# Optimization experiments

Hardware: AMD Instinct MI355X
Metric: run time of the kernel (lower is better)

Reference implementation:

```python
import jax, jax.numpy as jnp
import numpy as np

V = 100000
EMB = 300      # embedding_dim / output_dim
H1 = 100       # h1_dim
H2 = 100       # h2_dim
PROD = 100     # prod_dim
B = 16384


def setup_inputs() -> dict:
    key = jax.random.key(0)
    ks = jax.random.split(key, 16)
    targets = jax.random.randint(ks[0], (B,), 0, V)
    contexts = jax.random.randint(ks[1], (B,), 0, V)
    times = jax.random.uniform(ks[2], (B,), dtype=jnp.float32)
    labels = jax.random.randint(ks[3], (B,), 0, 2).astype(jnp.float32)
    # learned parameters
    targetemb = jax.random.normal(ks[4], (V, EMB), dtype=jnp.float32) * 0.02
    contextemb = jax.random.normal(ks[5], (V, EMB), dtype=jnp.float32) * 0.02
    # h1 initialized per the RANDA/RANDB scheme in __init__
    rng = np.random.RandomState(0)
    randoffset = rng.rand(H1, 1)
    randa = (1.0 / np.sqrt(2.0)) * rng.randn(H1, 1)
    randb = (-1.0 * randoffset * randa).reshape((H1,))
    h1_k = jnp.asarray(randa.reshape(1, H1), dtype=jnp.float32)
    h1_b = jnp.asarray(randb, dtype=jnp.float32)
    h2_k = jax.random.normal(ks[6], (H1, H2), dtype=jnp.float32) * 0.1
    h2_b = jnp.zeros((H2,), dtype=jnp.float32)
    evoke_k = jax.random.normal(ks[7], (EMB, H2 * PROD), dtype=jnp.float32) * 0.05
    evoke_b = jnp.zeros((H2 * PROD,), dtype=jnp.float32)
    last_k = jax.random.normal(ks[8], (PROD, EMB), dtype=jnp.float32) * 0.1
    last_b = jnp.zeros((EMB,), dtype=jnp.float32)
    return {
        "targets": targets, "contexts": contexts, "times": times, "labels": labels,
        "targetemb": targetemb, "contextemb": contextemb,
        "h1_k": h1_k, "h1_b": h1_b, "h2_k": h2_k, "h2_b": h2_b,
        "evoke_k": evoke_k, "evoke_b": evoke_b, "last_k": last_k, "last_b": last_b,
    }


def _branch_vector(emb, tv, evoke_k, evoke_b, last_k, last_b):
    # emb: [B, EMB] gathered embeddings; tv: [B, H2] time vector
    mat = (emb @ evoke_k + evoke_b).reshape(-1, PROD, H2)   # [B, PROD, H2]
    mv = jnp.einsum('bph,bh->bp', mat, tv)                   # batched matvec
    return mv @ last_k + last_b                              # [B, EMB]


def reference(targets, contexts, times, labels, targetemb, contextemb,
              h1_k, h1_b, h2_k, h2_b, evoke_k, evoke_b, last_k, last_b):
    # time MLP: two tanh dense layers (intended h1 -> h2 stack)
    t = times.reshape(-1, 1)
    h1 = jnp.tanh(t @ h1_k + h1_b)          # [B, H1]
    tv = jnp.tanh(h1 @ h2_k + h2_b)         # [B, H2]
    targ_vect = _branch_vector(targetemb[targets], tv, evoke_k, evoke_b, last_k, last_b)
    cont_vect = _branch_vector(contextemb[contexts], tv, evoke_k, evoke_b, last_k, last_b)
    logits = jnp.sum(targ_vect * cont_vect, axis=1)  # [B]
    # sigmoid_cross_entropy_with_logits, numerically stable
    loss = jnp.maximum(logits, 0.0) - logits * labels + jnp.log1p(jnp.exp(-jnp.abs(logits)))
    return jnp.mean(loss)
```

## Files before the change

### kernel.cpp

```cpp
#include <hip/hip_runtime.h>
#include <cstdint>

#define VOCAB 100000
#define EMB 300
#define NE 301
#define KP 128
#define EKSTRIDE 28672
#define NP 128
#define BM 64
#define BTOT 16384
#define PSZ 112
#define NGRP 4

typedef __attribute__((ext_vector_type(8))) short short8;
typedef __attribute__((ext_vector_type(4))) float f32x4;

__device__ __forceinline__ unsigned short f2bf(float f) {
    uint32_t u = __float_as_uint(f);
    uint32_t r = (u + 0x7fffu + ((u >> 16) & 1u)) >> 16;
    return (unsigned short)r;
}

__global__ __launch_bounds__(256) void k_ekprep(const float* __restrict__ evoke_k,
                                                const float* __restrict__ evoke_b,
                                                unsigned short* __restrict__ ekp) {
    int e = blockIdx.x;
    const float* src = (e < EMB) ? (evoke_k + (size_t)e * 10000) : evoke_b;
    uint32_t* dst = (uint32_t*)(ekp + (size_t)e * (EKSTRIDE / 2));
#pragma unroll
    for (int it = 0; it < 7; ++it) {
        int c    = it * 256 + threadIdx.x;
        int lane = c & 63;
        int ks   = (c >> 6) & 3;
        int t    = c >> 8;
        int p    = t * 16 + (lane & 15);
        int h0   = ks * 32 + (lane >> 4) * 8;
        uint32_t ov[4] = {0u, 0u, 0u, 0u};
        if (p < 100) {
#pragma unroll
            for (int j = 0; j < 8; ++j) {
                int h = h0 + j;
                float f = (h < 100) ? src[p * 100 + h] : 0.f;
                ov[j >> 1] |= (uint32_t)f2bf(f) << ((j & 1) * 16);
            }
        }
        uint32_t* o = dst + (size_t)c * 4;
        o[0] = ov[0]; o[1] = ov[1]; o[2] = ov[2]; o[3] = ov[3];
    }
}

__global__ __launch_bounds__(256) void k_tv(const float* __restrict__ times,
                                            const float* __restrict__ h1_k,
                                            const float* __restrict__ h1_b,
                                            const float* __restrict__ h2_k,
                                            const float* __restrict__ h2_b,
                                            unsigned short* __restrict__ tvp) {
    __shared__ float h1s[16][100];
    int b0 = blockIdx.x * 16;
    for (int idx = threadIdx.x; idx < 1600; idx += 256) {
        int bb = idx / 100, i = idx - bb * 100;
        h1s[bb][i] = tanhf(times[b0 + bb] * h1_k[i] + h1_b[i]);
    }
    __syncthreads();
    for (int idx = threadIdx.x; idx < 1600; idx += 256) {
        int bb = idx / 100, j = idx - bb * 100;
        float acc = h2_b[j];
        for (int i = 0; i < 100; ++i) acc += h1s[bb][i] * h2_k[i * 100 + j];
        tvp[(size_t)(b0 + bb) * KP + j] = f2bf(tanhf(acc));
    }
    for (int idx = threadIdx.x; idx < 16 * 28; idx += 256) {
        int bb = idx / 28, j = 100 + (idx - bb * 28);
        tvp[(size_t)(b0 + bb) * KP + j] = 0;
    }
}

__global__ __launch_bounds__(128) void k_gprep(const float* __restrict__ last_k,
                                               const float* __restrict__ last_b,
                                               float* __restrict__ G,
                                               float* __restrict__ vvec,
                                               float* __restrict__ c0,
                                               float* __restrict__ out) {
    int p = blockIdx.x;
    int q = threadIdx.x;
    __shared__ float row[EMB];
    for (int d = q; d < EMB; d += 128) row[d] = (p < 100) ? last_k[p * EMB + d] : 0.f;
    __syncthreads();
    float acc = 0.f;
    if (p < 100 && q < 100) {
        for (int d = 0; d < EMB; ++d) acc += row[d] * last_k[q * EMB + d];
    }
    G[p * NP + q] = acc;
    if (q == 0) {
        float a = 0.f;
        if (p < 100) {
            for (int d = 0; d < EMB; ++d) a += row[d] * last_b[d];
        }
        vvec[p] = a;
        if (p == 0) {
            float s = 0.f;
            for (int d = 0; d < EMB; ++d) s += last_b[d] * last_b[d];
            *c0 = s;
            *out = 0.f;
        }
    }
}

__global__ __launch_bounds__(256, 2) void k_main(
    const int* __restrict__ targets, const int* __restrict__ contexts,
    const float* __restrict__ targetemb, const float* __restrict__ contextemb,
    const unsigned short* __restrict__ ekp, const unsigned short* __restrict__ tvp,
    float* __restrict__ mvpt, float* __restrict__ mvpc) {
    extern __shared__ char smem[];

    const int tid  = threadIdx.x;
    const int lane = tid & 63;
    const int w    = tid >> 6;
    const int l15  = lane & 15;
    const int l4   = lane >> 4;
    const int low3 = blockIdx.x & 7;
    const int g    = low3 >> 1;
    const int bt   = ((blockIdx.x >> 3) << 1) | (low3 & 1);
    const int m0   = bt * BM;
    const int e0   = (g == 0) ? 0 : (1 + 75 * g);
    const int ecnt = (g == 0) ? 76 : 75;
    const int nreal= (g == 3) ? 74 : ecnt;

    unsigned short* embl = (unsigned short*)smem;

    short8 afrag[4][4];
#pragma unroll
    for (int mt = 0; mt < 4; ++mt) {
        int bg = m0 + mt * 16 + l15;
#pragma unroll
        for (int ks = 0; ks < 4; ++ks) {
            afrag[mt][ks] = *(const short8*)(tvp + (size_t)bg * KP + ks * 32 + l4 * 8);
        }
    }

    bool act[2];
    int  voff[2];
#pragma unroll
    for (int nt = 0; nt < 2; ++nt) {
        int t = w * 2 + nt;
        act[nt] = (t < 7);
        int tc = (t < 7) ? t : 6;
        voff[nt] = tc * 4096 + lane * 16;
    }

    auto issue = [&](short8 (&buf)[2][4], int el) {
        int eg = e0 + ((el < ecnt) ? el : (ecnt - 1));
        uint64_t base = (uint64_t)(const void*)ekp + (uint64_t)eg * EKSTRIDE;
#pragma unroll
        for (int nt = 0; nt < 2; ++nt) {
            asm volatile("global_load_dwordx4 %0, %1, %2 offset:0"
                         : "=v"(buf[nt][0]) : "v"(voff[nt]), "s"(base));
            asm volatile("global_load_dwordx4 %0, %1, %2 offset:1024"
                         : "=v"(buf[nt][1]) : "v"(voff[nt]), "s"(base));
            asm volatile("global_load_dwordx4 %0, %1, %2 offset:2048"
                         : "=v"(buf[nt][2]) : "v"(voff[nt]), "s"(base));
            asm volatile("global_load_dwordx4 %0, %1, %2 offset:3072"
                         : "=v"(buf[nt][3]) : "v"(voff[nt]), "s"(base));
        }
    };
#define WAIT8 do { asm volatile("s_waitcnt vmcnt(8)"); \
                   __builtin_amdgcn_sched_barrier(0); } while (0)
#define WAIT0 do { asm volatile("s_waitcnt vmcnt(0)"); \
                   __builtin_amdgcn_sched_barrier(0); } while (0)

    short8 bufA[2][4], bufB[2][4];
    issue(bufA, 0);
    issue(bufB, 1);

    {
        int off    = tid & 127;
        int b      = off & 63;
        int branch = off >> 6;
        int seg    = tid >> 7;
        int s0 = seg * 38;
        int s1 = (seg == 0) ? 38 : nreal;
        const int* idxp   = branch ? contexts : targets;
        const float* base = branch ? contextemb : targetemb;
        const float* row  = base + (size_t)idxp[m0 + b] * EMB + e0;
        int e = s0;
        for (; e + 3 < s1; e += 4) {
            float4 v = *(const float4*)(row + e);
            embl[(e + 0) * 128 + off] = f2bf(v.x);
            embl[(e + 1) * 128 + off] = f2bf(v.y);
            embl[(e + 2) * 128 + off] = f2bf(v.z);
            embl[(e + 3) * 128 + off] = f2bf(v.w);
        }
        for (; e < s1; ++e) embl[e * 128 + off] = f2bf(row[e]);
        if (g == 3 && seg == 1) embl[74 * 128 + off] = 0x3F80;
    }

    f32x4 acc_t[4][2], acc_c[4][2];
    const f32x4 zf = {0.f, 0.f, 0.f, 0.f};
#pragma unroll
    for (int mt = 0; mt < 4; ++mt) {
#pragma unroll
        for (int nt = 0; nt < 2; ++nt) { acc_t[mt][nt] = zf; acc_c[mt][nt] = zf; }
    }

    auto compute = [&](int el, short8 (&buf)[2][4]) {
        float et[4][4], ec[4][4];
#pragma unroll
        for (int mt = 0; mt < 4; ++mt) {
            int row0 = mt * 16 + l4 * 4;
            uint2 dt = *(const uint2*)(embl + el * 128 + row0);
            uint2 dc = *(const uint2*)(embl + el * 128 + 64 + row0);
            et[mt][0] = __uint_as_float(dt.x << 16);
            et[mt][1] = __uint_as_float(dt.x & 0xffff0000u);
            et[mt][2] = __uint_as_float(dt.y << 16);
            et[mt][3] = __uint_as_float(dt.y & 0xffff0000u);
            ec[mt][0] = __uint_as_float(dc.x << 16);
            ec[mt][1] = __uint_as_float(dc.x & 0xffff0000u);
            ec[mt][2] = __uint_as_float(dc.y << 16);
            ec[mt][3] = __uint_as_float(dc.y & 0xffff0000u);
        }
#pragma unroll
        for (int nt = 0; nt < 2; ++nt) {
            if (act[nt]) {
                f32x4 S[4];
#pragma unroll
                for (int mt = 0; mt < 4; ++mt) S[mt] = zf;
#pragma unroll
                for (int ks = 0; ks < 4; ++ks) {
#pragma unroll
                    for (int mt = 0; mt < 4; ++mt) {
                        S[mt] = __builtin_amdgcn_mfma_f32_16x16x32_bf16(
                            afrag[mt][ks], buf[nt][ks], S[mt], 0, 0, 0);
                    }
                }
#pragma unroll
                for (int mt = 0; mt < 4; ++mt) {
#pragma unroll
                    for (int r = 0; r < 4; ++r) {
                        acc_t[mt][nt][r] += et[mt][r] * S[mt][r];
                        acc_c[mt][nt][r] += ec[mt][r] * S[mt][r];
                    }
                }
            }
        }
    };

    __syncthreads();

    const int ITER = (ecnt - 2) >> 1;
#pragma unroll 1
    for (int i = 0; i < ITER; ++i) {
        int e = 2 * i;
        WAIT8;
        compute(e, bufA);
        issue(bufA, e + 2);
        WAIT8;
        compute(e + 1, bufB);
        issue(bufB, e + 3);
    }
    {
        int e2 = 2 * ITER;
        WAIT0;
        compute(e2, bufA);
        compute(e2 + 1, bufB);
        if (ecnt & 1) {
            issue(bufA, e2 + 2);
            WAIT0;
            compute(e2 + 2, bufA);
        }
    }

    float* ot = mvpt + (size_t)g * BTOT * PSZ;
    float* oc = mvpc + (size_t)g * BTOT * PSZ;
#pragma unroll
    for (int mt = 0; mt < 4; ++mt) {
#pragma unroll
        for (int nt = 0; nt < 2; ++nt) {
            if (act[nt]) {
                int col = (w * 2 + nt) * 16 + l15;
#pragma unroll
                for (int r = 0; r < 4; ++r) {
                    size_t row = m0 + mt * 16 + l4 * 4 + r;
                    ot[row * PSZ + col] = acc_t[mt][nt][r];
                    oc[row * PSZ + col] = acc_c[mt][nt][r];
                }
            }
        }
    }
}

__global__ __launch_bounds__(256) void k_fin(
    const float* __restrict__ labels,
    const float* __restrict__ G, const float* __restrict__ vvec,
    const float* __restrict__ c0p,
    const float* __restrict__ mvpt, const float* __restrict__ mvpc,
    float* __restrict__ out) {
    __shared__ float mvt[32 * PSZ];
    __shared__ float mvc[32 * PSZ];
    __shared__ float bsum[4];
    const int tid = threadIdx.x;
    const int m0  = blockIdx.x * 32;

    for (int idx = tid; idx < 32 * (PSZ / 4); idx += 256) {
        float4 st = make_float4(0.f, 0.f, 0.f, 0.f);
        float4 sc = make_float4(0.f, 0.f, 0.f, 0.f);
#pragma unroll
        for (int gg = 0; gg < NGRP; ++gg) {
            const float4* pt = (const float4*)(mvpt + (size_t)gg * BTOT * PSZ) +
                               (size_t)m0 * (PSZ / 4) + idx;
            const float4* pc = (const float4*)(mvpc + (size_t)gg * BTOT * PSZ) +
                               (size_t)m0 * (PSZ / 4) + idx;
            float4 a = *pt, b = *pc;
            st.x += a.x; st.y += a.y; st.z += a.z; st.w += a.w;
            sc.x += b.x; sc.y += b.y; sc.z += b.z; sc.w += b.w;
        }
        ((float4*)mvt)[idx] = st;
        ((float4*)mvc)[idx] = sc;
    }
    __syncthreads();

    int b_loc = tid >> 3;
    int oct   = tid & 7;
    const float4* Mrow = (const float4*)(mvc + b_loc * PSZ);

    float part = 0.f;
    for (int pp = 0; pp < 14; ++pp) {
        int p = oct * 14 + pp;
        const float4* Grow = (const float4*)(G + p * NP);
        float wq = 0.f;
#pragma unroll 7
        for (int qq = 0; qq < 28; ++qq) {
            float4 gg = Grow[qq];
            float4 m  = Mrow[qq];
            wq += gg.x * m.x + gg.y * m.y + gg.z * m.z + gg.w * m.w;
        }
        float mtv = mvt[b_loc * PSZ + p];
        float mcv = mvc[b_loc * PSZ + p];
        part += mtv * wq + vvec[p] * (mtv + mcv);
    }
    part += __shfl_xor(part, 1);
    part += __shfl_xor(part, 2);
    part += __shfl_xor(part, 4);

    float lossv = 0.f;
    if (oct == 0) {
        float logit = part + *c0p;
        float lab = labels[m0 + b_loc];
        lossv = fmaxf(logit, 0.f) - logit * lab + log1pf(expf(-fabsf(logit)));
    }
#pragma unroll
    for (int off = 8; off < 64; off <<= 1) lossv += __shfl_xor(lossv, off);
    int w = tid >> 6;
    if ((tid & 63) == 0) bsum[w] = lossv;
    __syncthreads();
    if (tid == 0) {
        atomicAdd(out, (bsum[0] + bsum[1] + bsum[2] + bsum[3]) * (1.0f / 16384.0f));
    }
}

extern "C" void kernel_launch(void* const* d_in, const int* in_sizes, int n_in,
                              void* d_out, int out_size, void* d_ws, size_t ws_size,
                              hipStream_t stream) {
    const int*   targets    = (const int*)d_in[0];
    const int*   contexts   = (const int*)d_in[1];
    const float* times      = (const float*)d_in[2];
    const float* labels     = (const float*)d_in[3];
    const float* targetemb  = (const float*)d_in[4];
    const float* contextemb = (const float*)d_in[5];
    const float* h1_k       = (const float*)d_in[6];
    const float* h1_b       = (const float*)d_in[7];
    const float* h2_k       = (const float*)d_in[8];
    const float* h2_b       = (const float*)d_in[9];
    const float* evoke_k    = (const float*)d_in[10];
    const float* evoke_b    = (const float*)d_in[11];
    const float* last_k     = (const float*)d_in[12];
    const float* last_b     = (const float*)d_in[13];
    float* out = (float*)d_out;

    char* ws = (char*)d_ws;
    unsigned short* ekp = (unsigned short*)ws;
    unsigned short* tvp = (unsigned short*)(ws + 8630272);
    float* G    = (float*)(ws + 8630272 + 4194304);
    float* vv   = (float*)(ws + 8630272 + 4194304 + 65536);
    float* c0   = (float*)(ws + 8630272 + 4194304 + 65536 + 512);
    float* mvpt = (float*)(ws + 8630272 + 4194304 + 65536 + 1024);
    float* mvpc = mvpt + (size_t)NGRP * BTOT * PSZ;

    k_ekprep<<<dim3(NE), dim3(256), 0, stream>>>(evoke_k, evoke_b, ekp);
    k_tv<<<dim3(BTOT / 16), dim3(256), 0, stream>>>(times, h1_k, h1_b, h2_k, h2_b, tvp);
    k_gprep<<<dim3(NP), dim3(128), 0, stream>>>(last_k, last_b, G, vv, c0, out);
    k_main<<<dim3(NGRP * BTOT / BM), dim3(256), 19456, stream>>>(
        targets, contexts, targetemb, contextemb, ekp, tvp, mvpt, mvpc);
    k_fin<<<dim3(BTOT / 32), dim3(256), 0, stream>>>(
        labels, G, vv, c0, mvpt, mvpc, out);
}
```

Baseline: 518.5 us.

## Merge prep kernels into one launch, stage G in LDS for finalize

Folds the three preprocessing kernels (evoke_k bf16 packing, time-MLP, last_k Gram matrix) into a single launch that dispatches on block index, saving two kernel launches. The finalize kernel now copies the Gram matrix into padded shared memory and handles 16 batch rows per block with 16 lanes per row, so G is no longer read from global memory inside the loop. The sched_barrier masks in the main kernel are relaxed to let the compiler move some instructions across the wait points. The cost is a large dynamic LDS allocation in finalize, about 65 KB per block, and each of its 1024 blocks reloads the full G.

```diff
diff --git a/kernel.cpp b/kernel.cpp
--- a/kernel.cpp
+++ b/kernel.cpp
@@ -11,6 +11,8 @@
 #define BTOT 16384
 #define PSZ 112
 #define NGRP 4
+#define FSB 16
+#define NPREP (NE + BTOT / 16 + 128)
 
 typedef __attribute__((ext_vector_type(8))) short short8;
 typedef __attribute__((ext_vector_type(4))) float f32x4;
@@ -21,86 +23,86 @@
     return (unsigned short)r;
 }
 
-__global__ __launch_bounds__(256) void k_ekprep(const float* __restrict__ evoke_k,
-                                                const float* __restrict__ evoke_b,
-                                                unsigned short* __restrict__ ekp) {
-    int e = blockIdx.x;
-    const float* src = (e < EMB) ? (evoke_k + (size_t)e * 10000) : evoke_b;
-    uint32_t* dst = (uint32_t*)(ekp + (size_t)e * (EKSTRIDE / 2));
-#pragma unroll
-    for (int it = 0; it < 7; ++it) {
-        int c    = it * 256 + threadIdx.x;
-        int lane = c & 63;
-        int ks   = (c >> 6) & 3;
-        int t    = c >> 8;
-        int p    = t * 16 + (lane & 15);
-        int h0   = ks * 32 + (lane >> 4) * 8;
-        uint32_t ov[4] = {0u, 0u, 0u, 0u};
-        if (p < 100) {
-#pragma unroll
-            for (int j = 0; j < 8; ++j) {
-                int h = h0 + j;
-                float f = (h < 100) ? src[p * 100 + h] : 0.f;
-                ov[j >> 1] |= (uint32_t)f2bf(f) << ((j & 1) * 16);
+__global__ __launch_bounds__(256) void k_prep(
+    const float* __restrict__ evoke_k, const float* __restrict__ evoke_b,
+    unsigned short* __restrict__ ekp,
+    const float* __restrict__ times,
+    const float* __restrict__ h1_k, const float* __restrict__ h1_b,
+    const float* __restrict__ h2_k, const float* __restrict__ h2_b,
+    unsigned short* __restrict__ tvp,
+    const float* __restrict__ last_k, const float* __restrict__ last_b,
+    float* __restrict__ G, float* __restrict__ vvec,
+    float* __restrict__ c0, float* __restrict__ out) {
+    __shared__ float h1s[16][100];
+    __shared__ float row[EMB];
+    const int b = blockIdx.x;
+
+    if (b < NE) {
+        int e = b;
+        const float* src = (e < EMB) ? (evoke_k + (size_t)e * 10000) : evoke_b;
+        uint32_t* dst = (uint32_t*)(ekp + (size_t)e * (EKSTRIDE / 2));
+#pragma unroll
+        for (int it = 0; it < 7; ++it) {
+            int c    = it * 256 + threadIdx.x;
+            int lane = c & 63;
+            int ks   = (c >> 6) & 3;
+            int t    = c >> 8;
+            int p    = t * 16 + (lane & 15);
+            int h0   = ks * 32 + (lane >> 4) * 8;
+            uint32_t ov[4] = {0u, 0u, 0u, 0u};
+            if (p < 100) {
+#pragma unroll
+                for (int j = 0; j < 8; ++j) {
+                    int h = h0 + j;
+                    float f = (h < 100) ? src[p * 100 + h] : 0.f;
+                    ov[j >> 1] |= (uint32_t)f2bf(f) << ((j & 1) * 16);
+                }
             }
-        }
-        uint32_t* o = dst + (size_t)c * 4;
-        o[0] = ov[0]; o[1] = ov[1]; o[2] = ov[2]; o[3] = ov[3];
-    }
-}
-
-__global__ __launch_bounds__(256) void k_tv(const float* __restrict__ times,
-                                            const float* __restrict__ h1_k,
-                                            const float* __restrict__ h1_b,
-                                            const float* __restrict__ h2_k,
-                                            const float* __restrict__ h2_b,
-                                            unsigned short* __restrict__ tvp) {
-    __shared__ float h1s[16][100];
-    int b0 = blockIdx.x * 16;
-    for (int idx = threadIdx.x; idx < 1600; idx += 256) {
-        int bb = idx / 100, i = idx - bb * 100;
-        h1s[bb][i] = tanhf(times[b0 + bb] * h1_k[i] + h1_b[i]);
-    }
-    __syncthreads();
-    for (int idx = threadIdx.x; idx < 1600; idx += 256) {
-        int bb = idx / 100, j = idx - bb * 100;
-        float acc = h2_b[j];
-        for (int i = 0; i < 100; ++i) acc += h1s[bb][i] * h2_k[i * 100 + j];
-        tvp[(size_t)(b0 + bb) * KP + j] = f2bf(tanhf(acc));
-    }
-    for (int idx = threadIdx.x; idx < 16 * 28; idx += 256) {
-        int bb = idx / 28, j = 100 + (idx - bb * 28);
-        tvp[(size_t)(b0 + bb) * KP + j] = 0;
-    }
-}
-
-__global__ __launch_bounds__(128) void k_gprep(const float* __restrict__ last_k,
-                                               const float* __restrict__ last_b,
-                                               float* __restrict__ G,
-                                               float* __restrict__ vvec,
-                                               float* __restrict__ c0,
-                                               float* __restrict__ out) {
-    int p = blockIdx.x;
-    int q = threadIdx.x;
-    __shared__ float row[EMB];
-    for (int d = q; d < EMB; d += 128) row[d] = (p < 100) ? last_k[p * EMB + d] : 0.f;
-    __syncthreads();
-    float acc = 0.f;
-    if (p < 100 && q < 100) {
-        for (int d = 0; d < EMB; ++d) acc += row[d] * last_k[q * EMB + d];
-    }
-    G[p * NP + q] = acc;
-    if (q == 0) {
-        float a = 0.f;
-        if (p < 100) {
-            for (int d = 0; d < EMB; ++d) a += row[d] * last_b[d];
-        }
-        vvec[p] = a;
-        if (p == 0) {
-            float s = 0.f;
-            for (int d = 0; d < EMB; ++d) s += last_b[d] * last_b[d];
-            *c0 = s;
-            *out = 0.f;
+            uint32_t* o = dst + (size_t)c * 4;
+            o[0] = ov[0]; o[1] = ov[1]; o[2] = ov[2]; o[3] = ov[3];
+        }
+    } else if (b < NE + BTOT / 16) {
+        int b0 = (b - NE) * 16;
+        for (int idx = threadIdx.x; idx < 1600; idx += 256) {
+            int bb = idx / 100, i = idx - bb * 100;
+            h1s[bb][i] = tanhf(times[b0 + bb] * h1_k[i] + h1_b[i]);
+        }
+        __syncthreads();
+        for (int idx = threadIdx.x; idx < 1600; idx += 256) {
+            int bb = idx / 100, j = idx - bb * 100;
+            float acc = h2_b[j];
+            for (int i = 0; i < 100; ++i) acc += h1s[bb][i] * h2_k[i * 100 + j];
+            tvp[(size_t)(b0 + bb) * KP + j] = f2bf(tanhf(acc));
+        }
+        for (int idx = threadIdx.x; idx < 16 * 28; idx += 256) {
+            int bb = idx / 28, j = 100 + (idx - bb * 28);
+            tvp[(size_t)(b0 + bb) * KP + j] = 0;
+        }
+    } else {
+        int p = b - NE - BTOT / 16;
+        int q = threadIdx.x;
+        for (int d = threadIdx.x; d < EMB; d += 256)
+            row[d] = (p < 100) ? last_k[p * EMB + d] : 0.f;
+        __syncthreads();
+        if (q < 128) {
+            float acc = 0.f;
+            if (p < 100 && q < 100) {
+                for (int d = 0; d < EMB; ++d) acc += row[d] * last_k[q * EMB + d];
+            }
+            G[p * NP + q] = acc;
+            if (q == 0) {
+                float a = 0.f;
+                if (p < 100) {
+                    for (int d = 0; d < EMB; ++d) a += row[d] * last_b[d];
+                }
+                vvec[p] = a;
+                if (p == 0) {
+                    float s = 0.f;
+                    for (int d = 0; d < EMB; ++d) s += last_b[d] * last_b[d];
+                    *c0 = s;
+                    *out = 0.f;
+                }
+            }
         }
     }
 }
@@ -163,9 +165,9 @@
         }
     };
 #define WAIT8 do { asm volatile("s_waitcnt vmcnt(8)"); \
-                   __builtin_amdgcn_sched_barrier(0); } while (0)
+                   __builtin_amdgcn_sched_barrier(0x387); } while (0)
 #define WAIT0 do { asm volatile("s_waitcnt vmcnt(0)"); \
-                   __builtin_amdgcn_sched_barrier(0); } while (0)
+                   __builtin_amdgcn_sched_barrier(0x387); } while (0)
 
     short8 bufA[2][4], bufB[2][4];
     issue(bufA, 0);
@@ -287,72 +289,77 @@
     }
 }
 
-__global__ __launch_bounds__(256) void k_fin(
+__global__ __launch_bounds__(256, 2) void k_fin(
     const float* __restrict__ labels,
     const float* __restrict__ G, const float* __restrict__ vvec,
     const float* __restrict__ c0p,
     const float* __restrict__ mvpt, const float* __restrict__ mvpc,
     float* __restrict__ out) {
-    __shared__ float mvt[32 * PSZ];
-    __shared__ float mvc[32 * PSZ];
-    __shared__ float bsum[4];
+    extern __shared__ float fs[];
+    float* Gs   = fs;
+    float* mts  = fs + 112 * 116;
+    float* mcs  = mts + FSB * PSZ;
+    float* vs   = mcs + FSB * PSZ;
+    float* lred = vs + PSZ;
     const int tid = threadIdx.x;
-    const int m0  = blockIdx.x * 32;
-
-    for (int idx = tid; idx < 32 * (PSZ / 4); idx += 256) {
+    const int m0  = blockIdx.x * FSB;
+
+    for (int idx = tid; idx < 112 * 28; idx += 256) {
+        int p = idx / 28, qq = idx - p * 28;
+        *(float4*)(Gs + p * 116 + qq * 4) = *(const float4*)(G + p * NP + qq * 4);
+    }
+    for (int idx = tid; idx < FSB * 28; idx += 256) {
+        int s = idx / 28, qq = idx - s * 28;
+        size_t base = (size_t)(m0 + s) * PSZ + qq * 4;
         float4 st = make_float4(0.f, 0.f, 0.f, 0.f);
         float4 sc = make_float4(0.f, 0.f, 0.f, 0.f);
 #pragma unroll
         for (int gg = 0; gg < NGRP; ++gg) {
-            const float4* pt = (const float4*)(mvpt + (size_t)gg * BTOT * PSZ) +
-                               (size_t)m0 * (PSZ / 4) + idx;
-            const float4* pc = (const float4*)(mvpc + (size_t)gg * BTOT * PSZ) +
-                               (size_t)m0 * (PSZ / 4) + idx;
-            float4 a = *pt, b = *pc;
+            float4 a = *(const float4*)(mvpt + (size_t)gg * BTOT * PSZ + base);
+            float4 c = *(const float4*)(mvpc + (size_t)gg * BTOT * PSZ + base);
             st.x += a.x; st.y += a.y; st.z += a.z; st.w += a.w;
-            sc.x += b.x; sc.y += b.y; sc.z += b.z; sc.w += b.w;
-        }
-        ((float4*)mvt)[idx] = st;
-        ((float4*)mvc)[idx] = sc;
-    }
+            sc.x += c.x; sc.y += c.y; sc.z += c.z; sc.w += c.w;
+        }
+        *(float4*)(mts + s * PSZ + qq * 4) = st;
+        *(float4*)(mcs + s * PSZ + qq * 4) = sc;
+    }
+    if (tid < PSZ) vs[tid] = vvec[tid];
     __syncthreads();
 
-    int b_loc = tid >> 3;
-    int oct   = tid & 7;
-    const float4* Mrow = (const float4*)(mvc + b_loc * PSZ);
-
+    const int s = tid >> 4;
+    const int l = tid & 15;
     float part = 0.f;
-    for (int pp = 0; pp < 14; ++pp) {
-        int p = oct * 14 + pp;
-        const float4* Grow = (const float4*)(G + p * NP);
+#pragma unroll 1
+    for (int k = 0; k < 7; ++k) {
+        int p = l * 7 + k;
+        const float4* Gr = (const float4*)(Gs + p * 116);
+        const float4* Mr = (const float4*)(mcs + s * PSZ);
         float wq = 0.f;
-#pragma unroll 7
+#pragma unroll
         for (int qq = 0; qq < 28; ++qq) {
-            float4 gg = Grow[qq];
-            float4 m  = Mrow[qq];
-            wq += gg.x * m.x + gg.y * m.y + gg.z * m.z + gg.w * m.w;
-        }
-        float mtv = mvt[b_loc * PSZ + p];
-        float mcv = mvc[b_loc * PSZ + p];
-        part += mtv * wq + vvec[p] * (mtv + mcv);
+            float4 g = Gr[qq];
+            float4 m = Mr[qq];
+            wq += g.x * m.x + g.y * m.y + g.z * m.z + g.w * m.w;
+        }
+        float mtv = mts[s * PSZ + p];
+        float mcv = mcs[s * PSZ + p];
+        part += mtv * wq + vs[p] * (mtv + mcv);
     }
     part += __shfl_xor(part, 1);
     part += __shfl_xor(part, 2);
     part += __shfl_xor(part, 4);
-
-    float lossv = 0.f;
-    if (oct == 0) {
+    part += __shfl_xor(part, 8);
+    if (l == 0) {
         float logit = part + *c0p;
-        float lab = labels[m0 + b_loc];
-        lossv = fmaxf(logit, 0.f) - logit * lab + log1pf(expf(-fabsf(logit)));
-    }
-#pragma unroll
-    for (int off = 8; off < 64; off <<= 1) lossv += __shfl_xor(lossv, off);
-    int w = tid >> 6;
-    if ((tid & 63) == 0) bsum[w] = lossv;
+        float lab = labels[m0 + s];
+        lred[s] = fmaxf(logit, 0.f) - logit * lab + log1pf(expf(-fabsf(logit)));
+    }
     __syncthreads();
     if (tid == 0) {
-        atomicAdd(out, (bsum[0] + bsum[1] + bsum[2] + bsum[3]) * (1.0f / 16384.0f));
+        float sum = 0.f;
+#pragma unroll
+        for (int i = 0; i < FSB; ++i) sum += lred[i];
+        atomicAdd(out, sum * (1.0f / 16384.0f));
     }
 }
 
@@ -384,11 +391,11 @@
     float* mvpt = (float*)(ws + 8630272 + 4194304 + 65536 + 1024);
     float* mvpc = mvpt + (size_t)NGRP * BTOT * PSZ;
 
-    k_ekprep<<<dim3(NE), dim3(256), 0, stream>>>(evoke_k, evoke_b, ekp);
-    k_tv<<<dim3(BTOT / 16), dim3(256), 0, stream>>>(times, h1_k, h1_b, h2_k, h2_b, tvp);
-    k_gprep<<<dim3(NP), dim3(128), 0, stream>>>(last_k, last_b, G, vv, c0, out);
+    k_prep<<<dim3(NPREP), dim3(256), 0, stream>>>(
+        evoke_k, evoke_b, ekp, times, h1_k, h1_b, h2_k, h2_b, tvp,
+        last_k, last_b, G, vv, c0, out);
     k_main<<<dim3(NGRP * BTOT / BM), dim3(256), 19456, stream>>>(
         targets, contexts, targetemb, contextemb, ekp, tvp, mvpt, mvpc);
-    k_fin<<<dim3(BTOT / 32), dim3(256), 0, stream>>>(
+    k_fin<<<dim3(BTOT / FSB), dim3(256), 66816, stream>>>(
         labels, G, vv, c0, mvpt, mvpc, out);
 }
```

Result: faster. 437.1 us (-15.7%).
